# Performance work log

Hardware: AMD Instinct MI355X
Metric: run time of the kernel (lower is better)

## Reference

```python
import jax, jax.numpy as jnp
import numpy as np
import math

HEADS = 8
DIM_HEAD = 64

def setup_inputs() -> dict:
    key = jax.random.key(0)
    ks = jax.random.split(key, 6)
    B, L, D = 2, 2048, 512
    Ls = 1936
    inner = HEADS * DIM_HEAD  # 512
    x = jax.random.normal(ks[0], (B, L, D), dtype=jnp.float32)
    positions = jax.random.normal(ks[1], (B, Ls, 2), dtype=jnp.float32) * 10.0
    w_qkv = jax.random.normal(ks[2], (3 * inner, D), dtype=jnp.float32) * (1.0 / math.sqrt(D))
    w_out = jax.random.normal(ks[3], (D, inner), dtype=jnp.float32) * (1.0 / math.sqrt(inner))
    b_out = jnp.zeros((D,), dtype=jnp.float32)
    log_sigma = jnp.full((HEADS,), math.log(3.0), dtype=jnp.float32)
    global_bias = jnp.float32(0.0)
    return {"x": x, "positions": positions, "w_qkv": w_qkv, "w_out": w_out,
            "b_out": b_out, "log_sigma": log_sigma, "global_bias": global_bias,
            "num_spatial": Ls}

def reference(x, positions, w_qkv, w_out, b_out, log_sigma, global_bias, num_spatial):
    B, L, D = x.shape
    H, Dh = HEADS, DIM_HEAD
    scale = Dh ** (-0.5)
    # qkv projection: [B,L,3*H*Dh] -> q,k,v each [B,H,L,Dh]
    qkv = jnp.einsum('bld,ed->ble', x, w_qkv)
    q, k, v = jnp.split(qkv, 3, axis=-1)
    def heads(t):
        return t.reshape(B, L, H, Dh).transpose(0, 2, 1, 3)
    q, k, v = heads(q), heads(k), heads(v)
    attn = jnp.einsum('bhid,bhjd->bhij', q, k) * scale  # [B,H,L,L]
    # Gaussian distance bias on the spatial block, global_bias elsewhere
    Ls = num_spatial
    diff = positions[:, :, None, :] - positions[:, None, :, :]  # [B,Ls,Ls,2]
    dist_sq = jnp.sum(diff * diff, axis=-1)                     # [B,Ls,Ls]
    sigma_sq = jnp.exp(log_sigma) ** 2                          # [H]
    spatial_bias = -dist_sq[:, None] / (2.0 * sigma_sq[None, :, None, None])  # [B,H,Ls,Ls]
    full_bias = jnp.full((B, H, L, L), global_bias, dtype=x.dtype)
    full_bias = full_bias.at[:, :, :Ls, :Ls].set(spatial_bias)
    attn = jax.nn.softmax(attn + full_bias, axis=-1)
    out = jnp.einsum('bhij,bhjd->bhid', attn, v)  # [B,H,L,Dh]
    out = out.transpose(0, 2, 1, 3).reshape(B, L, H * Dh)
    return jnp.einsum('ble,de->bld', out, w_out) + b_out
```

## Files before the change

kernel.cpp:

```cpp
#include <hip/hip_runtime.h>
#include <stdint.h>
#include <stddef.h>

#define NB   2
#define NL   2048
#define ND   512
#define NH   8
#define DH   64
#define LOG2E 1.44269504f
#define NIT  16
#define RG_TOT 32768

typedef __attribute__((ext_vector_type(8))) short bf16x8;
typedef __attribute__((ext_vector_type(4))) float f32x4;

__device__ __forceinline__ unsigned short f2bf(float f) {
  union { float f; unsigned int u; } c; c.f = f;
  unsigned int u = c.u;
  unsigned int r = u + 0x7fffu + ((u >> 16) & 1u);
  return (unsigned short)(r >> 16);
}

__device__ __forceinline__ float fexp2(float x) {
#if __has_builtin(__builtin_amdgcn_exp2f)
  return __builtin_amdgcn_exp2f(x);
#else
  return exp2f(x);
#endif
}

__device__ __forceinline__ void gl_lds16(const unsigned short* g, unsigned short* l) {
#if __has_builtin(__builtin_amdgcn_global_load_lds)
  __builtin_amdgcn_global_load_lds(
      (const __attribute__((address_space(1))) unsigned int*)g,
      (__attribute__((address_space(3))) unsigned int*)l, 16, 0, 0);
#else
  *(uint4*)l = *(const uint4*)g;
#endif
}

#define XC  524288
#define WQC 196608
#define WOC 65536
__global__ void cvt_f32_bf16(const float* __restrict__ x, const float* __restrict__ wq,
                             const float* __restrict__ wo, unsigned short* __restrict__ xb,
                             unsigned short* __restrict__ wqb, unsigned short* __restrict__ wob) {
  int idx = blockIdx.x * 256 + threadIdx.x;
  const float* src; unsigned short* dst; int off;
  if (idx < XC)            { src = x;  dst = xb;  off = idx; }
  else if (idx < XC + WQC) { src = wq; dst = wqb; off = idx - XC; }
  else                     { src = wo; dst = wob; off = idx - XC - WQC; }
  float4 f = ((const float4*)src)[off];
  ushort4 o;
  o.x = f2bf(f.x); o.y = f2bf(f.y); o.z = f2bf(f.z); o.w = f2bf(f.w);
  ((ushort4*)dst)[off] = o;
}

template<int MODE>
__global__ __launch_bounds__(256, 2) void gemm_bf16(
    const unsigned short* __restrict__ A, const unsigned short* __restrict__ Bm,
    const float* __restrict__ bias,
    unsigned short* __restrict__ qo, unsigned short* __restrict__ ko,
    unsigned short* __restrict__ vo, float* __restrict__ out, int K)
{
  __shared__ __align__(16) unsigned short As[128 * 32];
  __shared__ __align__(16) unsigned short Bs[128 * 32];
  const int tid = threadIdx.x, wid = tid >> 6, lane = tid & 63;
  const int quad = lane >> 4, l15 = lane & 15;
  const int m0 = blockIdx.x * 128, n0 = blockIdx.y * 128;
  const int wm = (wid >> 1) * 64, wn = (wid & 1) * 64;

  f32x4 acc[4][4];
#pragma unroll
  for (int a = 0; a < 4; ++a)
#pragma unroll
    for (int b = 0; b < 4; ++b)
#pragma unroll
      for (int z = 0; z < 4; ++z) acc[a][b][z] = 0.f;

  for (int k0 = 0; k0 < K; k0 += 32) {
#pragma unroll
    for (int p = 0; p < 2; ++p) {
      int c = p * 256 + wid * 64 + lane;
      int row = c >> 2, off = c & 3;
      gl_lds16(A  + (size_t)(m0 + row) * K + k0 + off * 8, &As[c * 8]);
      gl_lds16(Bm + (size_t)(n0 + row) * K + k0 + off * 8, &Bs[c * 8]);
    }
    __syncthreads();
    bf16x8 af[4], bfr[4];
#pragma unroll
    for (int mb = 0; mb < 4; ++mb)
      af[mb] = *(const bf16x8*)&As[(wm + mb * 16 + l15) * 32 + quad * 8];
#pragma unroll
    for (int nb = 0; nb < 4; ++nb)
      bfr[nb] = *(const bf16x8*)&Bs[(wn + nb * 16 + l15) * 32 + quad * 8];
#pragma unroll
    for (int mb = 0; mb < 4; ++mb)
#pragma unroll
      for (int nb = 0; nb < 4; ++nb)
        acc[mb][nb] = __builtin_amdgcn_mfma_f32_16x16x32_bf16(af[mb], bfr[nb], acc[mb][nb], 0, 0, 0);
    __syncthreads();
  }

  const float QSCALE = 0.125f * LOG2E;
#pragma unroll
  for (int mb = 0; mb < 4; ++mb) {
#pragma unroll
    for (int r = 0; r < 4; ++r) {
      int m  = m0 + wm + mb * 16 + quad * 4 + r;
      int bb = m >> 11;
      int ll = m & 2047;
#pragma unroll
      for (int nb = 0; nb < 4; ++nb) {
        int n = n0 + wn + nb * 16 + l15;
        float v = acc[mb][nb][r];
        if (MODE == 0) {
          int s  = n >> 9;
          int hh = (n >> 6) & 7;
          int dh = n & 63;
          size_t base = (((size_t)bb * NH + hh) * NL + ll) * DH + dh;
          if (s == 0)      qo[base] = f2bf(v * QSCALE);
          else if (s == 1) ko[base] = f2bf(v);
          else             vo[base] = f2bf(v);
        } else {
          out[(size_t)m * ND + n] = v + bias[n];
        }
      }
    }
  }
}

__global__ __launch_bounds__(256) void transpose_v(const unsigned short* __restrict__ v,
                                                   unsigned short* __restrict__ vT) {
  __shared__ unsigned short T[64][74];
  const int l0 = blockIdx.x * 64;
  const int bh = blockIdx.y;
  const unsigned short* src = v + ((size_t)bh * NL + l0) * DH;
  unsigned short* dst = vT + (size_t)bh * DH * NL;
#pragma unroll
  for (int p = 0; p < 2; ++p) {
    int c = p * 256 + threadIdx.x;
    int row = c >> 3, seg = c & 7;
    *(uint4*)&T[row][seg * 8] = *(const uint4*)(src + row * DH + seg * 8);
  }
  __syncthreads();
#pragma unroll
  for (int p = 0; p < 2; ++p) {
    int c = p * 256 + threadIdx.x;
    int drow = c >> 3, lseg = c & 7;
    unsigned short u[8];
#pragma unroll
    for (int z = 0; z < 8; ++z) u[z] = T[lseg * 8 + z][drow];
    *(uint4*)(dst + (size_t)drow * NL + l0 + lseg * 8) = *(uint4*)u;
  }
}

__global__ __launch_bounds__(256, 2) void flash_kernel(
    const unsigned short* __restrict__ qb, const unsigned short* __restrict__ kb,
    const unsigned short* __restrict__ vTb, const float* __restrict__ positions,
    const float* __restrict__ log_sigma, const float* __restrict__ gbias_p,
    const int* __restrict__ ns_p, float* __restrict__ Pbuf, float* __restrict__ rsbuf)
{
  const int it = blockIdx.x >> 1;
  const int js = blockIdx.x & 1;
  const int h  = blockIdx.y;
  const int b  = blockIdx.z;
  const int i0 = it * 128;
  const int jbase = js * (NL / 2);
  const int Ls = ns_p[0];
  const float gb = gbias_p[0];
  const float sig = __expf(log_sigma[h]);
  const float inv2s2 = 0.5f / (sig * sig);
  const float CI = LOG2E * inv2s2;
  const float A2 = 2.0f * CI;
  const float CG = LOG2E * gb * 0.5f;
  const float C8N = -8.0f * LOG2E;

  const int tid  = threadIdx.x;
  const int wid  = tid >> 6;
  const int lane = tid & 63;
  const int quad = lane >> 4;
  const int l15  = lane & 15;

  __shared__ __align__(16) unsigned short Ks[64][72];
  __shared__ __align__(16) unsigned short Vt[64][72];
  __shared__ __align__(16) unsigned short Ps[128][72];
  __shared__ __align__(16) float4 pjc[64];

  const size_t bh = (size_t)b * NH + h;
  const unsigned short* qbase  = qb  + (bh * NL + i0) * DH;
  const unsigned short* kbase  = kb  + bh * NL * DH;
  const unsigned short* vtbase = vTb + bh * DH * NL;

  bf16x8 af[2][2];
#pragma unroll
  for (int mb = 0; mb < 2; ++mb)
#pragma unroll
    for (int kc = 0; kc < 2; ++kc)
      af[mb][kc] = *(const bf16x8*)(qbase + (size_t)(wid * 32 + mb * 16 + l15) * DH + kc * 32 + quad * 8);

  float pix_[2][4], piy_[2][4], riCm[2][4], ispf[2][4];
#pragma unroll
  for (int mb = 0; mb < 2; ++mb)
#pragma unroll
    for (int r = 0; r < 4; ++r) {
      int ig = i0 + wid * 32 + mb * 16 + quad * 4 + r;
      float px = 0.f, py = 0.f, sf = 0.f, rc = 0.f;
      if (ig < Ls) {
        float2 p2 = *(const float2*)(positions + ((size_t)b * Ls + ig) * 2);
        px = p2.x; py = p2.y; sf = 1.f;
        rc = -(CI * (px * px + py * py)) - CG;
      }
      pix_[mb][r] = px; piy_[mb][r] = py; ispf[mb][r] = sf; riCm[mb][r] = rc;
    }

  f32x4 accO[2][4];
  float rsum[2][4];
#pragma unroll
  for (int mb = 0; mb < 2; ++mb) {
#pragma unroll
    for (int nb = 0; nb < 4; ++nb)
#pragma unroll
      for (int z = 0; z < 4; ++z) accO[mb][nb][z] = 0.f;
#pragma unroll
    for (int r = 0; r < 4; ++r) rsum[mb][r] = 0.f;
  }

  uint4 kr[2], vr[2];
  float2 pr = make_float2(0.f, 0.f);
  {
#pragma unroll
    for (int p = 0; p < 2; ++p) {
      int c = p * 256 + tid;
      int row = c >> 3, off = c & 7;
      kr[p] = *(const uint4*)(kbase  + (size_t)(jbase + row) * DH + off * 8);
      vr[p] = *(const uint4*)(vtbase + (size_t)row * NL + jbase + off * 8);
    }
    if (tid < 64 && (jbase + tid) < Ls)
      pr = *(const float2*)(positions + ((size_t)b * Ls + jbase + tid) * 2);
  }

  for (int jt = 0; jt < 16; ++jt) {
    const int j0 = jbase + jt * 64;
    __syncthreads();

#pragma unroll
    for (int p = 0; p < 2; ++p) {
      int c = p * 256 + tid;
      int row = c >> 3, off = c & 7;
      *(uint4*)&Ks[row][off * 8] = kr[p];
      *(uint4*)&Vt[row][off * 8] = vr[p];
    }
    if (tid < 64) {
      bool jsp = (j0 + tid) < Ls;
      float px = jsp ? pr.x : 0.f, py = jsp ? pr.y : 0.f;
      float rc = jsp ? (-(CI * (px * px + py * py)) - CG) : 0.f;
      pjc[tid] = make_float4(A2 * px, A2 * py, rc, 0.f);
    }
    __syncthreads();

    if (jt + 1 < 16) {
      const int jn = jbase + (jt + 1) * 64;
#pragma unroll
      for (int p = 0; p < 2; ++p) {
        int c = p * 256 + tid;
        int row = c >> 3, off = c & 7;
        kr[p] = *(const uint4*)(kbase  + (size_t)(jn + row) * DH + off * 8);
        vr[p] = *(const uint4*)(vtbase + (size_t)row * NL + jn + off * 8);
      }
      if (tid < 64 && (jn + tid) < Ls)
        pr = *(const float2*)(positions + ((size_t)b * Ls + jn + tid) * 2);
    }

    f32x4 accS[2][4];
#pragma unroll
    for (int mb = 0; mb < 2; ++mb)
#pragma unroll
      for (int nb = 0; nb < 4; ++nb)
#pragma unroll
        for (int z = 0; z < 4; ++z) accS[mb][nb][z] = 0.f;
#pragma unroll
    for (int nb = 0; nb < 4; ++nb) {
      bf16x8 b0 = *(const bf16x8*)&Ks[nb * 16 + l15][quad * 8];
      bf16x8 b1 = *(const bf16x8*)&Ks[nb * 16 + l15][32 + quad * 8];
#pragma unroll
      for (int mb = 0; mb < 2; ++mb) {
        accS[mb][nb] = __builtin_amdgcn_mfma_f32_16x16x32_bf16(af[mb][0], b0, accS[mb][nb], 0, 0, 0);
        accS[mb][nb] = __builtin_amdgcn_mfma_f32_16x16x32_bf16(af[mb][1], b1, accS[mb][nb], 0, 0, 0);
      }
    }

    float4 pc[4]; float jspf_[4];
#pragma unroll
    for (int nb = 0; nb < 4; ++nb) {
      pc[nb] = pjc[nb * 16 + l15];
      jspf_[nb] = ((j0 + nb * 16 + l15) < Ls) ? 1.f : 0.f;
    }
#pragma unroll
    for (int mb = 0; mb < 2; ++mb)
#pragma unroll
      for (int nb = 0; nb < 4; ++nb)
#pragma unroll
        for (int r = 0; r < 4; ++r) {
          float t = accS[mb][nb][r] + C8N;
          t = __builtin_fmaf(ispf[mb][r], pc[nb].z, t);
          t = __builtin_fmaf(jspf_[nb], riCm[mb][r], t);
          t = __builtin_fmaf(piy_[mb][r], pc[nb].y, t);
          t = __builtin_fmaf(pix_[mb][r], pc[nb].x, t);
          float p = fexp2(t);
          rsum[mb][r] += p;
          Ps[wid * 32 + mb * 16 + quad * 4 + r][nb * 16 + l15] = f2bf(p);
        }

    bf16x8 pf[2][2];
#pragma unroll
    for (int mb = 0; mb < 2; ++mb) {
      pf[mb][0] = *(const bf16x8*)&Ps[wid * 32 + mb * 16 + l15][quad * 8];
      pf[mb][1] = *(const bf16x8*)&Ps[wid * 32 + mb * 16 + l15][32 + quad * 8];
    }
#pragma unroll
    for (int nb = 0; nb < 4; ++nb) {
      bf16x8 v0 = *(const bf16x8*)&Vt[nb * 16 + l15][quad * 8];
      bf16x8 v1 = *(const bf16x8*)&Vt[nb * 16 + l15][32 + quad * 8];
#pragma unroll
      for (int mb = 0; mb < 2; ++mb) {
        accO[mb][nb] = __builtin_amdgcn_mfma_f32_16x16x32_bf16(pf[mb][0], v0, accO[mb][nb], 0, 0, 0);
        accO[mb][nb] = __builtin_amdgcn_mfma_f32_16x16x32_bf16(pf[mb][1], v1, accO[mb][nb], 0, 0, 0);
      }
    }
  }

#pragma unroll
  for (int mb = 0; mb < 2; ++mb)
#pragma unroll
    for (int r = 0; r < 4; ++r) {
      float v = rsum[mb][r];
      v += __shfl_xor(v, 1);
      v += __shfl_xor(v, 2);
      v += __shfl_xor(v, 4);
      v += __shfl_xor(v, 8);
      rsum[mb][r] = v;
    }
  const size_t rgbase = (bh * NIT + it) * 128;
  const size_t poff = (size_t)js * RG_TOT * DH;
#pragma unroll
  for (int mb = 0; mb < 2; ++mb)
#pragma unroll
    for (int r = 0; r < 4; ++r) {
      int row = wid * 32 + mb * 16 + quad * 4 + r;
#pragma unroll
      for (int nb = 0; nb < 4; ++nb)
        Pbuf[poff + (rgbase + row) * DH + nb * 16 + l15] = accO[mb][nb][r];
      if (l15 == 0)
        rsbuf[(size_t)js * RG_TOT + rgbase + row] = rsum[mb][r];
    }
}

__global__ __launch_bounds__(256) void combine_kernel(const float* __restrict__ Pbuf,
                                                      const float* __restrict__ rsbuf,
                                                      unsigned short* __restrict__ attnb) {
  int idx = blockIdx.x * 256 + threadIdx.x;
  int rg = idx >> 4, c4 = idx & 15;
  const float4* p4 = (const float4*)Pbuf;
  float4 p0 = p4[(size_t)rg * 16 + c4];
  float4 p1 = p4[(size_t)RG_TOT * 16 + (size_t)rg * 16 + c4];
  float rs = 1.0f / (rsbuf[rg] + rsbuf[RG_TOT + rg]);
  int bhm = rg >> 11;
  int l   = rg & 2047;
  int bb  = bhm >> 3, hh = bhm & 7;
  ushort4 o;
  o.x = f2bf((p0.x + p1.x) * rs);
  o.y = f2bf((p0.y + p1.y) * rs);
  o.z = f2bf((p0.z + p1.z) * rs);
  o.w = f2bf((p0.w + p1.w) * rs);
  *(ushort4*)&attnb[(((size_t)bb * NL + l) * ND) + hh * DH + c4 * 4] = o;
}

extern "C" void kernel_launch(void* const* d_in, const int* in_sizes, int n_in,
                              void* d_out, int out_size, void* d_ws, size_t ws_size,
                              hipStream_t stream) {
  const float* x         = (const float*)d_in[0];
  const float* positions = (const float*)d_in[1];
  const float* w_qkv     = (const float*)d_in[2];
  const float* w_out     = (const float*)d_in[3];
  const float* b_out     = (const float*)d_in[4];
  const float* log_sigma = (const float*)d_in[5];
  const float* gbias     = (const float*)d_in[6];
  const int*   ns        = (const int*)d_in[7];

  unsigned short* ws = (unsigned short*)d_ws;
  unsigned short* xb  = ws;
  unsigned short* wqb = xb  + 2097152;
  unsigned short* wob = wqb + 786432;
  unsigned short* qbf = wob + 262144;
  unsigned short* kbf = qbf + 2097152;
  unsigned short* vbf = kbf + 2097152;
  unsigned short* vTf = vbf + 2097152;
  float* Pbuf  = (float*)(vTf + 2097152);
  float* rsbuf = Pbuf + (size_t)2 * RG_TOT * DH;

  cvt_f32_bf16<<<(XC + WQC + WOC) / 256, 256, 0, stream>>>(x, w_qkv, w_out, xb, wqb, wob);

  dim3 g1(NB * NL / 128, (3 * NH * DH) / 128);
  gemm_bf16<0><<<g1, 256, 0, stream>>>(xb, wqb, nullptr, qbf, kbf, vbf, nullptr, ND);

  dim3 gt(NL / 64, NB * NH);
  transpose_v<<<gt, 256, 0, stream>>>(vbf, vTf);

  dim3 g2(NIT * 2, NH, NB);
  flash_kernel<<<g2, 256, 0, stream>>>(qbf, kbf, vTf, positions, log_sigma, gbias, ns,
                                       Pbuf, rsbuf);

  combine_kernel<<<RG_TOT * 16 / 256, 256, 0, stream>>>(Pbuf, rsbuf, xb);

  dim3 g3(NB * NL / 128, ND / 128);
  gemm_bf16<1><<<g3, 256, 0, stream>>>(xb, wob, b_out, nullptr, nullptr, nullptr,
                                       (float*)d_out, NH * DH);
}
```

Before: 167.1 us.

## Fuse V transpose into QKV GEMM, split keys four ways, store partials in bf16

The QKV GEMM now computes the transposed product (weights times tokens), so its epilogue writes Q and K with vector stores and writes V directly in transposed layout. That removes the separate transpose kernel and the extra V buffer. The flash kernel splits the key dimension into 4 chunks instead of 2, giving four times as many blocks, and writes partial outputs as bf16 rather than fp32. The combine kernel sums the four partials. The output GEMM uses a 64-row tile and vectorized bias-add stores, and the workspace is aliased so the weight copy shares space with the partial buffers. In exchange, the bf16 partials lose some precision, and the V epilogue issues scattered 2-byte stores.

```diff
diff --git a/kernel.cpp b/kernel.cpp
--- a/kernel.cpp
+++ b/kernel.cpp
@@ -10,6 +10,7 @@
 #define LOG2E 1.44269504f
 #define NIT  16
 #define RG_TOT 32768
+#define JS   4
 
 typedef __attribute__((ext_vector_type(8))) short bf16x8;
 typedef __attribute__((ext_vector_type(4))) float f32x4;
@@ -19,6 +20,10 @@
   unsigned int u = c.u;
   unsigned int r = u + 0x7fffu + ((u >> 16) & 1u);
   return (unsigned short)(r >> 16);
+}
+
+__device__ __forceinline__ float bf2f(unsigned short u) {
+  union { unsigned int i; float f; } c; c.i = ((unsigned int)u) << 16; return c.f;
 }
 
 __device__ __forceinline__ float fexp2(float x) {
@@ -42,6 +47,7 @@
 #define XC  524288
 #define WQC 196608
 #define WOC 65536
+#define TOTC (XC + WQC + WOC)
 __global__ void cvt_f32_bf16(const float* __restrict__ x, const float* __restrict__ wq,
                              const float* __restrict__ wo, unsigned short* __restrict__ xb,
                              unsigned short* __restrict__ wqb, unsigned short* __restrict__ wob) {
@@ -56,23 +62,25 @@
   ((ushort4*)dst)[off] = o;
 }
 
-template<int MODE>
+template<int MODE, int MT>
 __global__ __launch_bounds__(256, 2) void gemm_bf16(
     const unsigned short* __restrict__ A, const unsigned short* __restrict__ Bm,
     const float* __restrict__ bias,
     unsigned short* __restrict__ qo, unsigned short* __restrict__ ko,
-    unsigned short* __restrict__ vo, float* __restrict__ out, int K)
+    unsigned short* __restrict__ vTo, float* __restrict__ out, int K)
 {
-  __shared__ __align__(16) unsigned short As[128 * 32];
-  __shared__ __align__(16) unsigned short Bs[128 * 32];
+  constexpr int MB = MT / 32;
+  constexpr int AC = MT * 4;
+  constexpr int TC = AC + 512;
+  __shared__ __align__(16) unsigned short S[MT * 32 + 128 * 32];
   const int tid = threadIdx.x, wid = tid >> 6, lane = tid & 63;
   const int quad = lane >> 4, l15 = lane & 15;
-  const int m0 = blockIdx.x * 128, n0 = blockIdx.y * 128;
-  const int wm = (wid >> 1) * 64, wn = (wid & 1) * 64;
-
-  f32x4 acc[4][4];
-#pragma unroll
-  for (int a = 0; a < 4; ++a)
+  const int m0 = blockIdx.x * MT, n0 = blockIdx.y * 128;
+  const int wm = (wid >> 1) * (MT / 2), wn = (wid & 1) * 64;
+
+  f32x4 acc[MB][4];
+#pragma unroll
+  for (int a = 0; a < MB; ++a)
 #pragma unroll
     for (int b = 0; b < 4; ++b)
 #pragma unroll
@@ -80,22 +88,27 @@
 
   for (int k0 = 0; k0 < K; k0 += 32) {
 #pragma unroll
-    for (int p = 0; p < 2; ++p) {
+    for (int p = 0; p < TC / 256; ++p) {
       int c = p * 256 + wid * 64 + lane;
-      int row = c >> 2, off = c & 3;
-      gl_lds16(A  + (size_t)(m0 + row) * K + k0 + off * 8, &As[c * 8]);
-      gl_lds16(Bm + (size_t)(n0 + row) * K + k0 + off * 8, &Bs[c * 8]);
+      if (c < AC) {
+        int row = c >> 2, off = c & 3;
+        gl_lds16(A + (size_t)(m0 + row) * K + k0 + off * 8, &S[c * 8]);
+      } else {
+        int cb = c - AC;
+        int row = cb >> 2, off = cb & 3;
+        gl_lds16(Bm + (size_t)(n0 + row) * K + k0 + off * 8, &S[c * 8]);
+      }
     }
     __syncthreads();
-    bf16x8 af[4], bfr[4];
-#pragma unroll
-    for (int mb = 0; mb < 4; ++mb)
-      af[mb] = *(const bf16x8*)&As[(wm + mb * 16 + l15) * 32 + quad * 8];
+    bf16x8 af[MB], bfr[4];
+#pragma unroll
+    for (int mb = 0; mb < MB; ++mb)
+      af[mb] = *(const bf16x8*)&S[(wm + mb * 16 + l15) * 32 + quad * 8];
 #pragma unroll
     for (int nb = 0; nb < 4; ++nb)
-      bfr[nb] = *(const bf16x8*)&Bs[(wn + nb * 16 + l15) * 32 + quad * 8];
-#pragma unroll
-    for (int mb = 0; mb < 4; ++mb)
+      bfr[nb] = *(const bf16x8*)&S[MT * 32 + (wn + nb * 16 + l15) * 32 + quad * 8];
+#pragma unroll
+    for (int mb = 0; mb < MB; ++mb)
 #pragma unroll
       for (int nb = 0; nb < 4; ++nb)
         acc[mb][nb] = __builtin_amdgcn_mfma_f32_16x16x32_bf16(af[mb], bfr[nb], acc[mb][nb], 0, 0, 0);
@@ -104,54 +117,50 @@
 
   const float QSCALE = 0.125f * LOG2E;
 #pragma unroll
-  for (int mb = 0; mb < 4; ++mb) {
-#pragma unroll
-    for (int r = 0; r < 4; ++r) {
-      int m  = m0 + wm + mb * 16 + quad * 4 + r;
-      int bb = m >> 11;
-      int ll = m & 2047;
+  for (int mb = 0; mb < MB; ++mb) {
+    int e0 = m0 + wm + mb * 16 + quad * 4;
+    if (MODE == 0) {
+      int s   = e0 >> 9;
+      int hh  = (e0 >> 6) & 7;
+      int dh0 = e0 & 63;
+      if (s < 2) {
+        unsigned short* dst = (s == 0) ? qo : ko;
+        float sc = (s == 0) ? QSCALE : 1.0f;
+#pragma unroll
+        for (int nb = 0; nb < 4; ++nb) {
+          int token = n0 + wn + nb * 16 + l15;
+          int bb = token >> 11, ll = token & 2047;
+          ushort4 o;
+          o.x = f2bf(acc[mb][nb][0] * sc);
+          o.y = f2bf(acc[mb][nb][1] * sc);
+          o.z = f2bf(acc[mb][nb][2] * sc);
+          o.w = f2bf(acc[mb][nb][3] * sc);
+          *(ushort4*)&dst[(((size_t)bb * NH + hh) * NL + ll) * DH + dh0] = o;
+        }
+      } else {
+#pragma unroll
+        for (int nb = 0; nb < 4; ++nb) {
+          int token = n0 + wn + nb * 16 + l15;
+          int bb = token >> 11, ll = token & 2047;
+          size_t base = ((size_t)bb * NH + hh) * DH * NL + ll;
+#pragma unroll
+          for (int r = 0; r < 4; ++r)
+            vTo[base + (size_t)(dh0 + r) * NL] = f2bf(acc[mb][nb][r]);
+        }
+      }
+    } else {
+      float4 bv = *(const float4*)&bias[e0];
 #pragma unroll
       for (int nb = 0; nb < 4; ++nb) {
-        int n = n0 + wn + nb * 16 + l15;
-        float v = acc[mb][nb][r];
-        if (MODE == 0) {
-          int s  = n >> 9;
-          int hh = (n >> 6) & 7;
-          int dh = n & 63;
-          size_t base = (((size_t)bb * NH + hh) * NL + ll) * DH + dh;
-          if (s == 0)      qo[base] = f2bf(v * QSCALE);
-          else if (s == 1) ko[base] = f2bf(v);
-          else             vo[base] = f2bf(v);
-        } else {
-          out[(size_t)m * ND + n] = v + bias[n];
-        }
-      }
-    }
-  }
-}
-
-__global__ __launch_bounds__(256) void transpose_v(const unsigned short* __restrict__ v,
-                                                   unsigned short* __restrict__ vT) {
-  __shared__ unsigned short T[64][74];
-  const int l0 = blockIdx.x * 64;
-  const int bh = blockIdx.y;
-  const unsigned short* src = v + ((size_t)bh * NL + l0) * DH;
-  unsigned short* dst = vT + (size_t)bh * DH * NL;
-#pragma unroll
-  for (int p = 0; p < 2; ++p) {
-    int c = p * 256 + threadIdx.x;
-    int row = c >> 3, seg = c & 7;
-    *(uint4*)&T[row][seg * 8] = *(const uint4*)(src + row * DH + seg * 8);
-  }
-  __syncthreads();
-#pragma unroll
-  for (int p = 0; p < 2; ++p) {
-    int c = p * 256 + threadIdx.x;
-    int drow = c >> 3, lseg = c & 7;
-    unsigned short u[8];
-#pragma unroll
-    for (int z = 0; z < 8; ++z) u[z] = T[lseg * 8 + z][drow];
-    *(uint4*)(dst + (size_t)drow * NL + l0 + lseg * 8) = *(uint4*)u;
+        int token = n0 + wn + nb * 16 + l15;
+        float4 o;
+        o.x = acc[mb][nb][0] + bv.x;
+        o.y = acc[mb][nb][1] + bv.y;
+        o.z = acc[mb][nb][2] + bv.z;
+        o.w = acc[mb][nb][3] + bv.w;
+        *(float4*)&out[(size_t)token * ND + e0] = o;
+      }
+    }
   }
 }
 
@@ -159,19 +168,18 @@
     const unsigned short* __restrict__ qb, const unsigned short* __restrict__ kb,
     const unsigned short* __restrict__ vTb, const float* __restrict__ positions,
     const float* __restrict__ log_sigma, const float* __restrict__ gbias_p,
-    const int* __restrict__ ns_p, float* __restrict__ Pbuf, float* __restrict__ rsbuf)
+    const int* __restrict__ ns_p, unsigned short* __restrict__ Pb, float* __restrict__ rsbuf)
 {
-  const int it = blockIdx.x >> 1;
-  const int js = blockIdx.x & 1;
+  const int it = blockIdx.x >> 2;
+  const int js = blockIdx.x & 3;
   const int h  = blockIdx.y;
   const int b  = blockIdx.z;
   const int i0 = it * 128;
-  const int jbase = js * (NL / 2);
+  const int jbase = js * (NL / JS);
   const int Ls = ns_p[0];
   const float gb = gbias_p[0];
   const float sig = __expf(log_sigma[h]);
-  const float inv2s2 = 0.5f / (sig * sig);
-  const float CI = LOG2E * inv2s2;
+  const float CI = LOG2E * 0.5f / (sig * sig);
   const float A2 = 2.0f * CI;
   const float CG = LOG2E * gb * 0.5f;
   const float C8N = -8.0f * LOG2E;
@@ -240,7 +248,7 @@
       pr = *(const float2*)(positions + ((size_t)b * Ls + jbase + tid) * 2);
   }
 
-  for (int jt = 0; jt < 16; ++jt) {
+  for (int jt = 0; jt < NL / JS / 64; ++jt) {
     const int j0 = jbase + jt * 64;
     __syncthreads();
 
@@ -259,7 +267,7 @@
     }
     __syncthreads();
 
-    if (jt + 1 < 16) {
+    if (jt + 1 < NL / JS / 64) {
       const int jn = jbase + (jt + 1) * 64;
 #pragma unroll
       for (int p = 0; p < 2; ++p) {
@@ -350,29 +358,33 @@
       int row = wid * 32 + mb * 16 + quad * 4 + r;
 #pragma unroll
       for (int nb = 0; nb < 4; ++nb)
-        Pbuf[poff + (rgbase + row) * DH + nb * 16 + l15] = accO[mb][nb][r];
+        Pb[poff + (rgbase + row) * DH + nb * 16 + l15] = f2bf(accO[mb][nb][r]);
       if (l15 == 0)
         rsbuf[(size_t)js * RG_TOT + rgbase + row] = rsum[mb][r];
     }
 }
 
-__global__ __launch_bounds__(256) void combine_kernel(const float* __restrict__ Pbuf,
+__global__ __launch_bounds__(256) void combine_kernel(const unsigned short* __restrict__ Pb,
                                                       const float* __restrict__ rsbuf,
                                                       unsigned short* __restrict__ attnb) {
   int idx = blockIdx.x * 256 + threadIdx.x;
   int rg = idx >> 4, c4 = idx & 15;
-  const float4* p4 = (const float4*)Pbuf;
-  float4 p0 = p4[(size_t)rg * 16 + c4];
-  float4 p1 = p4[(size_t)RG_TOT * 16 + (size_t)rg * 16 + c4];
-  float rs = 1.0f / (rsbuf[rg] + rsbuf[RG_TOT + rg]);
+  float s0 = 0.f, s1 = 0.f, s2 = 0.f, s3 = 0.f, rsum = 0.f;
+#pragma unroll
+  for (int js = 0; js < JS; ++js) {
+    ushort4 u = *(const ushort4*)&Pb[((size_t)js * RG_TOT + rg) * DH + c4 * 4];
+    s0 += bf2f(u.x); s1 += bf2f(u.y); s2 += bf2f(u.z); s3 += bf2f(u.w);
+    rsum += rsbuf[(size_t)js * RG_TOT + rg];
+  }
+  float rs = 1.0f / rsum;
   int bhm = rg >> 11;
   int l   = rg & 2047;
   int bb  = bhm >> 3, hh = bhm & 7;
   ushort4 o;
-  o.x = f2bf((p0.x + p1.x) * rs);
-  o.y = f2bf((p0.y + p1.y) * rs);
-  o.z = f2bf((p0.z + p1.z) * rs);
-  o.w = f2bf((p0.w + p1.w) * rs);
+  o.x = f2bf(s0 * rs);
+  o.y = f2bf(s1 * rs);
+  o.z = f2bf(s2 * rs);
+  o.w = f2bf(s3 * rs);
   *(ushort4*)&attnb[(((size_t)bb * NL + l) * ND) + hh * DH + c4 * 4] = o;
 }
 
@@ -388,32 +400,29 @@
   const float* gbias     = (const float*)d_in[6];
   const int*   ns        = (const int*)d_in[7];
 
-  unsigned short* ws = (unsigned short*)d_ws;
+  unsigned short* ws  = (unsigned short*)d_ws;
   unsigned short* xb  = ws;
-  unsigned short* wqb = xb  + 2097152;
-  unsigned short* wob = wqb + 786432;
+  unsigned short* wob = xb  + 2097152;
   unsigned short* qbf = wob + 262144;
   unsigned short* kbf = qbf + 2097152;
-  unsigned short* vbf = kbf + 2097152;
-  unsigned short* vTf = vbf + 2097152;
-  float* Pbuf  = (float*)(vTf + 2097152);
-  float* rsbuf = Pbuf + (size_t)2 * RG_TOT * DH;
-
-  cvt_f32_bf16<<<(XC + WQC + WOC) / 256, 256, 0, stream>>>(x, w_qkv, w_out, xb, wqb, wob);
-
-  dim3 g1(NB * NL / 128, (3 * NH * DH) / 128);
-  gemm_bf16<0><<<g1, 256, 0, stream>>>(xb, wqb, nullptr, qbf, kbf, vbf, nullptr, ND);
-
-  dim3 gt(NL / 64, NB * NH);
-  transpose_v<<<gt, 256, 0, stream>>>(vbf, vTf);
-
-  dim3 g2(NIT * 2, NH, NB);
+  unsigned short* vTf = kbf + 2097152;
+  unsigned short* R   = vTf + 2097152;
+  unsigned short* wqb = R;
+  unsigned short* Pb  = R;
+  float* rsbuf = (float*)(Pb + (size_t)JS * RG_TOT * DH);
+
+  cvt_f32_bf16<<<TOTC / 256, 256, 0, stream>>>(x, w_qkv, w_out, xb, wqb, wob);
+
+  dim3 g1((3 * NH * DH) / 128, NB * NL / 128);
+  gemm_bf16<0, 128><<<g1, 256, 0, stream>>>(wqb, xb, nullptr, qbf, kbf, vTf, nullptr, ND);
+
+  dim3 g2((NL / 128) * JS, NH, NB);
   flash_kernel<<<g2, 256, 0, stream>>>(qbf, kbf, vTf, positions, log_sigma, gbias, ns,
-                                       Pbuf, rsbuf);
-
-  combine_kernel<<<RG_TOT * 16 / 256, 256, 0, stream>>>(Pbuf, rsbuf, xb);
-
-  dim3 g3(NB * NL / 128, ND / 128);
-  gemm_bf16<1><<<g3, 256, 0, stream>>>(xb, wob, b_out, nullptr, nullptr, nullptr,
-                                       (float*)d_out, NH * DH);
-}
+                                       Pb, rsbuf);
+
+  combine_kernel<<<RG_TOT * 16 / 256, 256, 0, stream>>>(Pb, rsbuf, xb);
+
+  dim3 g3(ND / 64, NB * NL / 128);
+  gemm_bf16<1, 64><<<g3, 256, 0, stream>>>(wob, xb, b_out, nullptr, nullptr, nullptr,
+                                           (float*)d_out, NH * DH);
+}
```

New measurement: 169.8 us. No clear change (+1.6%).
